# Performance work log

Measured on AMD Instinct MI355X. Metric: run time of the kernel, lower is better.

Reference implementation:

```python
import jax, jax.numpy as jnp
import numpy as np

NUM_CLASSES = 1000
MOMENTUM = 0.9
EPSILON = 1e-6
N = 65536


def setup_inputs() -> dict:
    key = jax.random.key(0)
    k1, k2 = jax.random.split(key)
    logits = jax.random.normal(k1, (N, NUM_CLASSES), dtype=jnp.float32)
    targets = jax.random.randint(k2, (N,), 0, NUM_CLASSES, dtype=jnp.int64)
    grad_mag = jnp.ones((NUM_CLASSES,), dtype=jnp.float32)  # buffer init = ones
    return {"logits": logits, "targets": targets, "grad_mag": grad_mag}


def reference(logits, targets, grad_mag):
    n = logits.shape[0]
    # per-sample cross entropy, reduction='none'
    logp = jax.nn.log_softmax(logits, axis=-1)  # [N, C]
    ce = -jnp.take_along_axis(logp, targets[:, None], axis=-1)[:, 0]  # [N]

    # per-class mean CE via one segment-reduce pass (replaces the Python loop)
    sums = jax.ops.segment_sum(ce, targets, num_segments=NUM_CLASSES)  # [C]
    counts = jax.ops.segment_sum(jnp.ones_like(ce), targets, num_segments=NUM_CLASSES)
    class_mean = jnp.abs(sums / jnp.maximum(counts, 1.0))

    # EMA update only for classes present in the batch (mask.any())
    present = counts > 0
    new_gm = jnp.where(present,
                       MOMENTUM * grad_mag + (1.0 - MOMENTUM) * class_mean,
                       grad_mag)  # [C]

    # inverse-magnitude weights, renormalized to sum to N
    w = 1.0 / (new_gm[targets] + EPSILON)  # [N]
    w = w / jnp.sum(w) * n
    return jnp.mean(w * ce)
```

## Files before the change

kernel.cpp:

```cpp
#include <hip/hip_runtime.h>
#include <math.h>

#define NUM_C   1000
#define MOM     0.9f
#define EPS     1e-6f

__global__ __launch_bounds__(256) void ce_kernel(const float* __restrict__ logits,
                                                 const int*   __restrict__ targets,
                                                 float* __restrict__ sums,
                                                 float* __restrict__ counts,
                                                 int n) {
    const int wave = threadIdx.x >> 6;
    const int lane = threadIdx.x & 63;
    const int row  = blockIdx.x * 4 + wave;
    if (row >= n) return;

    const int t  = targets[row];
    const int tq = t >> 2;
    const int tc = t & 3;

    const float4* rp = reinterpret_cast<const float4*>(logits + (size_t)row * NUM_C);

    float4 v[4];
    float m = -INFINITY;
#pragma unroll
    for (int j = 0; j < 4; ++j) {
        int idx = j * 64 + lane;
        if (idx < 250) {
            v[j] = rp[idx];
            m = fmaxf(m, fmaxf(fmaxf(v[j].x, v[j].y), fmaxf(v[j].z, v[j].w)));
        }
    }
#pragma unroll
    for (int off = 32; off > 0; off >>= 1)
        m = fmaxf(m, __shfl_xor(m, off, 64));

    float s = 0.f;
    float lt = 0.f;
#pragma unroll
    for (int j = 0; j < 4; ++j) {
        int idx = j * 64 + lane;
        if (idx < 250) {
            s += __expf(v[j].x - m);
            s += __expf(v[j].y - m);
            s += __expf(v[j].z - m);
            s += __expf(v[j].w - m);
            if (idx == tq) {
                float c = (tc == 0) ? v[j].x : (tc == 1) ? v[j].y
                        : (tc == 2) ? v[j].z : v[j].w;
                lt = c;
            }
        }
    }
#pragma unroll
    for (int off = 32; off > 0; off >>= 1) {
        s  += __shfl_xor(s,  off, 64);
        lt += __shfl_xor(lt, off, 64);
    }

    if (lane == 0) {
        float ce = (m + __logf(s)) - lt;
        atomicAdd(&sums[t], ce);
        atomicAdd(&counts[t], 1.0f);
    }
}

__global__ __launch_bounds__(1024) void finalize_kernel(const float* __restrict__ gm_in,
                                                        const float* __restrict__ sums,
                                                        const float* __restrict__ counts,
                                                        float* __restrict__ out) {
    const int c = threadIdx.x;
    float a = 0.f, b = 0.f;
    if (c < NUM_C) {
        float cnt = counts[c];
        float s   = sums[c];
        float g   = gm_in[c];
        if (cnt > 0.f) {
            float cm = fabsf(s / fmaxf(cnt, 1.0f));
            g = MOM * g + (1.0f - MOM) * cm;
        }
        float w = 1.0f / (g + EPS);
        a = cnt * w;
        b = s * w;
    }
#pragma unroll
    for (int off = 32; off > 0; off >>= 1) {
        a += __shfl_xor(a, off, 64);
        b += __shfl_xor(b, off, 64);
    }
    __shared__ float sa[16], sb[16];
    const int lane = threadIdx.x & 63;
    const int wv   = threadIdx.x >> 6;
    if (lane == 0) { sa[wv] = a; sb[wv] = b; }
    __syncthreads();
    if (threadIdx.x == 0) {
        float A = 0.f, B = 0.f;
        for (int i = 0; i < 16; ++i) { A += sa[i]; B += sb[i]; }
        out[0] = B / A;
    }
}

extern "C" void kernel_launch(void* const* d_in, const int* in_sizes, int n_in,
                              void* d_out, int out_size, void* d_ws, size_t ws_size,
                              hipStream_t stream) {
    const float* logits  = (const float*)d_in[0];
    const int*   targets = (const int*)d_in[1];
    const float* gm      = (const float*)d_in[2];
    float* out = (float*)d_out;

    const int n = in_sizes[1];

    float* sums   = (float*)d_ws;
    float* counts = sums + NUM_C;

    hipMemsetAsync(sums, 0, 2 * NUM_C * sizeof(float), stream);

    ce_kernel<<<(n + 3) / 4, 256, 0, stream>>>(logits, targets, sums, counts, n);
    finalize_kernel<<<1, 1024, 0, stream>>>(gm, sums, counts, out);
}
```

Measured before the change: 52.84 us.

## Replace global atomic class histogram with per-row CE buffer and LDS reduction

The CE kernel now writes each row's loss to a workspace array instead of issuing two global float atomics per row into 1000 class bins. The single-block finalize kernel reads targets and losses vectorised and builds the per-class sums and counts with shared-memory atomics, so the memset launch is no longer needed. This removes contended global atomics and one launch, but moves a serial 65536-element pass onto a single workgroup.

```diff
diff --git a/kernel.cpp b/kernel.cpp
--- a/kernel.cpp
+++ b/kernel.cpp
@@ -7,8 +7,7 @@
 
 __global__ __launch_bounds__(256) void ce_kernel(const float* __restrict__ logits,
                                                  const int*   __restrict__ targets,
-                                                 float* __restrict__ sums,
-                                                 float* __restrict__ counts,
+                                                 float* __restrict__ ce,
                                                  int n) {
     const int wave = threadIdx.x >> 6;
     const int lane = threadIdx.x & 63;
@@ -46,9 +45,8 @@
             s += __expf(v[j].z - m);
             s += __expf(v[j].w - m);
             if (idx == tq) {
-                float c = (tc == 0) ? v[j].x : (tc == 1) ? v[j].y
-                        : (tc == 2) ? v[j].z : v[j].w;
-                lt = c;
+                lt = (tc == 0) ? v[j].x : (tc == 1) ? v[j].y
+                   : (tc == 2) ? v[j].z : v[j].w;
             }
         }
     }
@@ -58,22 +56,42 @@
         lt += __shfl_xor(lt, off, 64);
     }
 
-    if (lane == 0) {
-        float ce = (m + __logf(s)) - lt;
-        atomicAdd(&sums[t], ce);
-        atomicAdd(&counts[t], 1.0f);
-    }
+    if (lane == 0)
+        ce[row] = (m + __logf(s)) - lt;
 }
 
-__global__ __launch_bounds__(1024) void finalize_kernel(const float* __restrict__ gm_in,
-                                                        const float* __restrict__ sums,
-                                                        const float* __restrict__ counts,
-                                                        float* __restrict__ out) {
+__global__ __launch_bounds__(1024) void finalize_kernel(const int*   __restrict__ targets,
+                                                        const float* __restrict__ ce,
+                                                        const float* __restrict__ gm_in,
+                                                        float* __restrict__ out,
+                                                        int n) {
+    __shared__ float ls[NUM_C];
+    __shared__ float lc[NUM_C];
+    for (int c = threadIdx.x; c < NUM_C; c += 1024) { ls[c] = 0.f; lc[c] = 0.f; }
+    __syncthreads();
+
+    const int nq = n >> 2;
+    const int4*   tp = reinterpret_cast<const int4*>(targets);
+    const float4* cp = reinterpret_cast<const float4*>(ce);
+    for (int i = threadIdx.x; i < nq; i += 1024) {
+        int4   t4 = tp[i];
+        float4 c4 = cp[i];
+        atomicAdd(&ls[t4.x], c4.x); atomicAdd(&lc[t4.x], 1.0f);
+        atomicAdd(&ls[t4.y], c4.y); atomicAdd(&lc[t4.y], 1.0f);
+        atomicAdd(&ls[t4.z], c4.z); atomicAdd(&lc[t4.z], 1.0f);
+        atomicAdd(&ls[t4.w], c4.w); atomicAdd(&lc[t4.w], 1.0f);
+    }
+    for (int i = (nq << 2) + (int)threadIdx.x; i < n; i += 1024) {
+        int t = targets[i];
+        atomicAdd(&ls[t], ce[i]); atomicAdd(&lc[t], 1.0f);
+    }
+    __syncthreads();
+
     const int c = threadIdx.x;
     float a = 0.f, b = 0.f;
     if (c < NUM_C) {
-        float cnt = counts[c];
-        float s   = sums[c];
+        float cnt = lc[c];
+        float s   = ls[c];
         float g   = gm_in[c];
         if (cnt > 0.f) {
             float cm = fabsf(s / fmaxf(cnt, 1.0f));
@@ -110,11 +128,8 @@
 
     const int n = in_sizes[1];
 
-    float* sums   = (float*)d_ws;
-    float* counts = sums + NUM_C;
+    float* ce = (float*)d_ws;
 
-    hipMemsetAsync(sums, 0, 2 * NUM_C * sizeof(float), stream);
-
-    ce_kernel<<<(n + 3) / 4, 256, 0, stream>>>(logits, targets, sums, counts, n);
-    finalize_kernel<<<1, 1024, 0, stream>>>(gm, sums, counts, out);
+    ce_kernel<<<(n + 3) / 4, 256, 0, stream>>>(logits, targets, ce, n);
+    finalize_kernel<<<1, 1024, 0, stream>>>(targets, ce, gm, out, n);
 }
```

Measured after the change: 207.7 us. +293.0%, slower.
